# Kernel optimization log

Measured on AMD Instinct MI355X. Metric: run time of the kernel, lower is better.

## Reference

```python
import jax, jax.numpy as jnp
import numpy as np

N_WIRES = 12
N_QLAYERS = 2
DIM = 2 ** N_WIRES


def setup_inputs() -> dict:
    key = jax.random.key(0)
    k0, k1, k2, k3 = jax.random.split(key, 4)
    x = jax.random.normal(k0, (2048, 1024), dtype=jnp.float32)
    # TT cores: ranks [1,16,1], input dims [32,32], output dims [8,9]
    core0 = jax.random.normal(k1, (1, 32, 8, 16), dtype=jnp.float32) * 0.05
    core1 = jax.random.normal(k2, (16, 32, 9, 1), dtype=jnp.float32) * 0.05
    tt_bias = jnp.zeros((72,), dtype=jnp.float32)
    global_angles = jax.random.normal(k3, (N_QLAYERS, N_WIRES, 3), dtype=jnp.float32) * 0.1
    return {"x": x, "core0": core0, "core1": core1, "tt_bias": tt_bias,
            "global_angles": global_angles}


def _rot(angles):
    # angles [..., 3] -> combined U = Rz @ Ry @ Rx, shape [..., 2, 2] complex64
    half = angles * 0.5
    cx, sx = jnp.cos(half[..., 0]), jnp.sin(half[..., 0])
    cy, sy = jnp.cos(half[..., 1]), jnp.sin(half[..., 1])
    cz, sz = jnp.cos(half[..., 2]), jnp.sin(half[..., 2])
    zero = jnp.zeros_like(cx)
    cplx = jax.lax.complex
    Rx = jnp.stack([jnp.stack([cplx(cx, zero), cplx(zero, -sx)], -1),
                    jnp.stack([cplx(zero, -sx), cplx(cx, zero)], -1)], -2)
    Ry = jnp.stack([jnp.stack([cplx(cy, zero), cplx(-sy, zero)], -1),
                    jnp.stack([cplx(sy, zero), cplx(cy, zero)], -1)], -2)
    ez, ezc = cplx(cz, -sz), cplx(cz, sz)  # exp(-i z/2), exp(+i z/2)
    zc = cplx(zero, zero)
    Rz = jnp.stack([jnp.stack([ez, zc], -1), jnp.stack([zc, ezc], -1)], -2)
    return jnp.einsum('...ij,...jk,...kl->...il', Rz, Ry, Rx)


def _apply_1q(state, U, w):
    # state [bsz, 2^n]; U [bsz, 2, 2]; wire 0 = most significant qubit
    bsz = state.shape[0]
    left, right = 2 ** w, 2 ** (N_WIRES - w - 1)
    s = state.reshape(bsz, left, 2, right)
    s = jnp.einsum('bij,bljr->blir', U, s)
    return s.reshape(bsz, DIM)


def _cnot(state, c, t):
    bsz = state.shape[0]
    s = state.reshape((bsz,) + (2,) * N_WIRES)
    s0 = jax.lax.index_in_dim(s, 0, c + 1, keepdims=True)
    s1 = jax.lax.index_in_dim(s, 1, c + 1, keepdims=True)
    s1 = jnp.flip(s1, axis=t + 1)  # flip target amplitudes where control = 1
    return jnp.concatenate([s0, s1], axis=c + 1).reshape(bsz, DIM)


def reference(x, core0, core1, tt_bias, global_angles):
    bsz = x.shape[0]
    # --- TT layer: x[b,32,32] contracted with two TT cores -> [b,8,9] -> [b,72]
    x_rs = x.reshape(bsz, 32, 32)
    tt_out = jnp.einsum('bij,aipq,qjrs->bpr', x_rs, core0, core1).reshape(bsz, -1) + tt_bias
    # residual global angles
    angles = global_angles[None, :, :, :] + tt_out.reshape(bsz, N_QLAYERS, N_WIRES, 3)
    U = _rot(angles)  # [bsz, L, n, 2, 2]
    # --- tensor-product Ry encoding of x[:, :n_wires] on |0...0>
    enc = x[:, :N_WIRES] * 0.5
    amp = jnp.stack([jnp.cos(enc), jnp.sin(enc)], -1)  # [bsz, n, 2]
    state = amp[:, 0, :]
    for w in range(1, N_WIRES):
        state = (state[:, :, None] * amp[:, w, None, :]).reshape(bsz, -1)
    state = state.astype(jnp.complex64)  # [bsz, 2^n]
    # --- VQC layers: fused Rz@Ry@Rx per wire, then ring CNOT (noise_prob=0)
    for k in range(N_QLAYERS):
        for w in range(N_WIRES):
            state = _apply_1q(state, U[:, k, w], w)
        for i in range(N_WIRES - 1):
            state = _cnot(state, i, i + 1)
        state = _cnot(state, N_WIRES - 1, 0)
    # --- MeasureAll(PauliZ): <Z_w> per wire
    probs = jnp.real(state * jnp.conj(state))  # [bsz, 2^n]
    idx = jnp.arange(DIM)[:, None]
    bits = (idx >> jnp.arange(N_WIRES - 1, -1, -1)[None, :]) & 1  # [2^n, n]
    zsign = (1.0 - 2.0 * bits).astype(jnp.float32)
    return probs @ zsign  # [bsz, n_wires]
```

## Files before the change

kernel.cpp:

```cpp
#include <hip/hip_runtime.h>
#include <math.h>

#define N_WIRES 12

__host__ __device__ constexpr int parity12(int x) {
  x ^= x >> 8; x ^= x >> 4; x ^= x >> 2; x ^= x >> 1;
  return x & 1;
}

__host__ __device__ constexpr int lanemask_of(int m) {
  return (((m >> 9) & 1) << 0) | (((m >> 8) & 1) << 1) |
         (((m >> 7) & 1) << 2) | (((m >> 6) & 1) << 3) |
         (((m >> 5) & 1) << 4) | (((m >> 11) & 1) << 5);
}

typedef float2 f2;
__device__ __forceinline__ f2 mk2(float a, float b) { f2 r; r.x = a; r.y = b; return r; }
__device__ __forceinline__ f2 pkmul(f2 a, f2 b) {
  f2 d; asm("v_pk_mul_f32 %0, %1, %2" : "=v"(d) : "v"(a), "v"(b)); return d;
}
__device__ __forceinline__ f2 pkfma(f2 a, f2 b, f2 c) {
  f2 d; asm("v_pk_fma_f32 %0, %1, %2, %3" : "=v"(d) : "v"(a), "v"(b), "v"(c)); return d;
}
__device__ __forceinline__ f2 swap2(f2 v) { return mk2(v.y, v.x); }

struct cpx { float r, i; };
__device__ __forceinline__ cpx cmulc(cpx a, cpx b) {
  return {a.r * b.r - a.i * b.i, a.r * b.i + a.i * b.r};
}
__device__ __forceinline__ cpx fpick(float r0, float i0, float r1, float i1, int b) {
  cpx c; c.r = b ? r1 : r0; c.i = b ? i1 : i0; return c;
}
__device__ __forceinline__ float rl(float v, int l) {
  return __int_as_float(__builtin_amdgcn_readlane(__float_as_int(v), l));
}

template <int CTRL>
__device__ __forceinline__ float dppmov(float v) {
  return __int_as_float(
      __builtin_amdgcn_mov_dpp(__float_as_int(v), CTRL, 0xF, 0xF, true));
}

template <int LM>
__device__ __forceinline__ float lshfl(float v) {
  if constexpr (LM == 0) {
    return v;
  } else if constexpr (LM == 0x01) {
    return dppmov<0xB1>(v);
  } else if constexpr (LM == 0x02) {
    return dppmov<0x4E>(v);
  } else if constexpr (LM == 0x03) {
    return dppmov<0x1B>(v);
  } else if constexpr (LM == 0x04) {
    return dppmov<0x1B>(dppmov<0x141>(v));
  } else if constexpr (LM == 0x07) {
    return dppmov<0x141>(v);
  } else if constexpr (LM == 0x08) {
    return dppmov<0x141>(dppmov<0x140>(v));
  } else if constexpr (LM == 0x0F) {
    return dppmov<0x140>(v);
  } else if constexpr ((LM & 0x30) != 0) {
    return lshfl<LM & 0x0F>(__shfl_xor(v, LM & 0x30, 64));
  } else {
    return __shfl_xor(v, LM, 64);
  }
}
template <int LM>
__device__ __forceinline__ f2 lshfl2(f2 v) {
  return mk2(lshfl<LM>(v.x), lshfl<LM>(v.y));
}

__global__ __launch_bounds__(256) void build_w_kernel(
    const float* __restrict__ core0,
    const float* __restrict__ core1,
    float* __restrict__ Wt) {
  int idx = blockIdx.x * 256 + threadIdx.x;
  int k = idx / 72;
  int o = idx - k * 72;
  int i = k >> 5, jj = k & 31;
  int p = o / 9, r = o - p * 9;
  float acc = 0.f;
#pragma unroll
  for (int q = 0; q < 16; ++q) {
    acc += core0[(i * 8 + p) * 16 + q] * core1[(q * 32 + jj) * 9 + r];
  }
  int og = o / 9, j = o - og * 9;
  Wt[k * 96 + og * 12 + j] = acc;
}

__global__ __launch_bounds__(512, 2) void tt_gemm4(
    const float* __restrict__ x,
    const float* __restrict__ Wt,
    const float* __restrict__ bias,
    float* __restrict__ ttout) {
  __shared__ __align__(16) float ws[128 * 100];
  __shared__ __align__(16) float xs[8 * 132];
  const int t = threadIdx.x;
  const int lane = t & 63;
  const int og = t >> 6;
  const int kk = lane & 15;
  const int rq = lane >> 4;
  const int row0 = blockIdx.x * 8;

  float a0[9], a1[9];
#pragma unroll
  for (int j = 0; j < 9; ++j) { a0[j] = 0.f; a1[j] = 0.f; }

  for (int s = 0; s < 8; ++s) {
    __syncthreads();
    const float4* Wg = (const float4*)(Wt + (size_t)s * 128 * 96);
#pragma unroll
    for (int i = 0; i < 6; ++i) {
      const int idx = i * 512 + t;
      const int r = idx / 24, c = idx - r * 24;
      *(float4*)&ws[r * 100 + c * 4] = Wg[idx];
    }
    if (t < 256) {
      const int rr = t >> 5, j4 = t & 31;
      *(float4*)&xs[rr * 132 + j4 * 4] =
          *(const float4*)(x + (size_t)(row0 + rr) * 1024 + s * 128 + j4 * 4);
    }
    __syncthreads();
#pragma unroll
    for (int i = 0; i < 8; ++i) {
      const int k = kk + i * 16;
      const float4 wA = *(const float4*)&ws[k * 100 + og * 12];
      const float4 wB = *(const float4*)&ws[k * 100 + og * 12 + 4];
      const float w8 = ws[k * 100 + og * 12 + 8];
      const float x0v = xs[(rq * 2) * 132 + k];
      const float x1v = xs[(rq * 2 + 1) * 132 + k];
      a0[0] += x0v * wA.x; a0[1] += x0v * wA.y;
      a0[2] += x0v * wA.z; a0[3] += x0v * wA.w;
      a0[4] += x0v * wB.x; a0[5] += x0v * wB.y;
      a0[6] += x0v * wB.z; a0[7] += x0v * wB.w;
      a0[8] += x0v * w8;
      a1[0] += x1v * wA.x; a1[1] += x1v * wA.y;
      a1[2] += x1v * wA.z; a1[3] += x1v * wA.w;
      a1[4] += x1v * wB.x; a1[5] += x1v * wB.y;
      a1[6] += x1v * wB.z; a1[7] += x1v * wB.w;
      a1[8] += x1v * w8;
    }
  }

#pragma unroll
  for (int j = 0; j < 9; ++j) {
    a0[j] += lshfl<0x01>(a0[j]);
    a0[j] += lshfl<0x02>(a0[j]);
    a0[j] += lshfl<0x04>(a0[j]);
    a0[j] += lshfl<0x08>(a0[j]);
    a1[j] += lshfl<0x01>(a1[j]);
    a1[j] += lshfl<0x02>(a1[j]);
    a1[j] += lshfl<0x04>(a1[j]);
    a1[j] += lshfl<0x08>(a1[j]);
  }
  if (kk == 0) {
#pragma unroll
    for (int j = 0; j < 9; ++j) {
      const float bj = bias[og * 9 + j];
      ttout[(size_t)(row0 + rq * 2) * 72 + og * 9 + j] = a0[j] + bj;
      ttout[(size_t)(row0 + rq * 2 + 1) * 72 + og * 9 + j] = a1[j] + bj;
    }
  }
}

template <int MASK, int ROW>
__device__ __forceinline__ void gate9(f2 R[16], f2 I[16],
    float u00r, float u00i, float u01r, float u01i,
    f2* __restrict__ buf, int t, int lane, int wq) {
  constexpr int RM   = MASK & 0x1F;
  constexpr int LMP  = lanemask_of(MASK);
  constexpr int WB   = (MASK >> 10) & 1;
  constexpr int ROWL = lanemask_of(ROW);
  constexpr int RWB  = (ROW >> 10) & 1;
  constexpr int FLIP = parity12(ROW & 3);
  constexpr int JX = (RM == 0) ? 0 : (((RM & 1) ? (RM ^ 3) : RM) >> 1);
  constexpr bool SW = (RM & 1) != 0;

  const int tsgn = ((__popc(ROWL & lane) ^ (RWB & wq)) & 1) << 31;
  const float dEi = __int_as_float(__float_as_int(u00i) ^ tsgn);
  const float oEr = __int_as_float(__float_as_int(u01r) ^ tsgn);
  const float ndEi = -dEi, noEr = -oEr;
  const f2 A  = mk2(u00r, u00r);
  const f2 C  = mk2(u01i, u01i);
  const f2 nC = mk2(-u01i, -u01i);

  auto Dof = [&](int pe, int ph) { return mk2(pe ? ndEi : dEi, ph ? ndEi : dEi); };
  auto Oof = [&](int pe, int ph) { return mk2(pe ? noEr : oEr, ph ? noEr : oEr); };

  auto upd = [&](int j, f2 Rb, f2 Ib, f2& outR, f2& outI) {
    const int pe = parity12(ROW & (2 * j));
    const int ph = pe ^ FLIP;
    const f2 Dj = Dof(pe, ph), nDj = Dof(!pe, !ph), Oj = Oof(pe, ph);
    const f2 a = R[j], ii = I[j];
    outR = pkfma(A, a, pkfma(nDj, ii, pkfma(Oj, Rb, pkmul(nC, Ib))));
    outI = pkfma(Dj, a, pkfma(A, ii, pkfma(C, Rb, pkmul(Oj, Ib))));
  };

  if constexpr (WB) {
    static_assert(RM == 0, "wave-crossing gate must have no reg part");
    const int tp = t ^ 64 ^ LMP;
#pragma unroll
    for (int ph2 = 0; ph2 < 2; ++ph2) {
      __syncthreads();
#pragma unroll
      for (int j = 0; j < 8; ++j) {
        buf[(j * 2 + 0) * 256 + t] = R[ph2 * 8 + j];
        buf[(j * 2 + 1) * 256 + t] = I[ph2 * 8 + j];
      }
      __syncthreads();
#pragma unroll
      for (int j = 0; j < 8; ++j) {
        const f2 Rb = buf[(j * 2 + 0) * 256 + tp];
        const f2 Ib = buf[(j * 2 + 1) * 256 + tp];
        upd(ph2 * 8 + j, Rb, Ib, R[ph2 * 8 + j], I[ph2 * 8 + j]);
      }
    }
  } else if constexpr (LMP != 0 && RM == 0) {
#pragma unroll
    for (int j = 0; j < 16; ++j) {
      const f2 Rb = lshfl2<LMP>(R[j]);
      const f2 Ib = lshfl2<LMP>(I[j]);
      f2 nR, nI;
      upd(j, Rb, Ib, nR, nI);
      R[j] = nR; I[j] = nI;
    }
  } else if constexpr (LMP != 0 && RM != 0) {
#pragma unroll
    for (int j = 0; j < 16; ++j) {
      const int j2 = j ^ JX;
      if (j < j2) {
        f2 Rb1 = lshfl2<LMP>(R[j2]), Ib1 = lshfl2<LMP>(I[j2]);
        f2 Rb2 = lshfl2<LMP>(R[j]),  Ib2 = lshfl2<LMP>(I[j]);
        if constexpr (SW) {
          Rb1 = swap2(Rb1); Ib1 = swap2(Ib1);
          Rb2 = swap2(Rb2); Ib2 = swap2(Ib2);
        }
        f2 nR1, nI1, nR2, nI2;
        upd(j, Rb1, Ib1, nR1, nI1);
        upd(j2, Rb2, Ib2, nR2, nI2);
        R[j] = nR1; I[j] = nI1; R[j2] = nR2; I[j2] = nI2;
      }
    }
  } else {
#pragma unroll
    for (int j = 0; j < 16; ++j) {
      const int j2 = j ^ JX;
      if (j < j2) {
        f2 Rb1 = R[j2], Ib1 = I[j2], Rb2 = R[j], Ib2 = I[j];
        if constexpr (SW) {
          Rb1 = swap2(Rb1); Ib1 = swap2(Ib1);
          Rb2 = swap2(Rb2); Ib2 = swap2(Ib2);
        }
        f2 nR1, nI1, nR2, nI2;
        upd(j, Rb1, Ib1, nR1, nI1);
        upd(j2, Rb2, Ib2, nR2, nI2);
        R[j] = nR1; I[j] = nI1; R[j2] = nR2; I[j2] = nI2;
      }
    }
  }
}

__global__ __launch_bounds__(256, 3) void vqc_kernel10(
    const float* __restrict__ x,
    const float* __restrict__ ttout,
    const float* __restrict__ gang,
    float* __restrict__ out) {
  const int t = threadIdx.x;
  const int lane = t & 63;
  const int wq = (t >> 6) & 1;
  const int row = t >> 7;
  const int b = blockIdx.x * 2 + row;
  const float* ttb = ttout + (size_t)b * 72;

  __shared__ __align__(16) f2 buf[4096];

  float c0 = 0.f, c1 = 0.f, c2 = 0.f, c3 = 0.f;
  const bool uLane = lane < 12;
  const bool fLane = (lane >= 16) && (lane < 28);
  if (uLane || fLane) {
    const int w = uLane ? lane : lane - 16;
    const int k = uLane ? 1 : 0;
    const int gbase = (k * 12 + w) * 3;
    const int tbase = k * 36 + w * 3;
    const float a0 = gang[gbase + 0] + ttb[tbase + 0];
    const float a1 = gang[gbase + 1] + ttb[tbase + 1];
    const float a2 = gang[gbase + 2] + ttb[tbase + 2];
    const float cx = cosf(0.5f * a0), sx = sinf(0.5f * a0);
    const float cy = cosf(0.5f * a1), sy = sinf(0.5f * a1);
    const float cz = cosf(0.5f * a2), sz = sinf(0.5f * a2);
    const float m00r = cy * cx,   m00i = sy * sx;
    const float m01r = -sy * cx,  m01i = -cy * sx;
    const float m10r = sy * cx,   m10i = -cy * sx;
    const float m11r = cy * cx,   m11i = -sy * sx;
    const float U00r = cz * m00r + sz * m00i, U00i = cz * m00i - sz * m00r;
    const float U01r = cz * m01r + sz * m01i, U01i = cz * m01i - sz * m01r;
    const float U10r = cz * m10r - sz * m10i, U10i = cz * m10i + sz * m10r;
    const float U11r = cz * m11r - sz * m11i, U11i = cz * m11i + sz * m11r;
    if (uLane) {
      c0 = U00r; c1 = U00i; c2 = U01r; c3 = U01i;
    } else {
      const float e = x[(size_t)b * 1024 + w] * 0.5f;
      const float cc = cosf(e), ss = sinf(e);
      c0 = U00r * cc + U01r * ss;  c1 = U00i * cc + U01i * ss;
      c2 = U10r * cc + U11r * ss;  c3 = U10i * cc + U11i * ss;
    }
  }

  const int bw0 = (lane >> 5) & 1;
  const int bw1 = (wq ^ lane) & 1;
  const int bw2 = (lane ^ (lane >> 1)) & 1;
  const int bw3 = ((lane >> 1) ^ (lane >> 2)) & 1;
  const int bw4 = ((lane >> 2) ^ (lane >> 3)) & 1;
  const int bw5 = ((lane >> 3) ^ (lane >> 4)) & 1;
  const int l4 = (lane >> 4) & 1;

  cpx P = fpick(rl(c0, 16), rl(c1, 16), rl(c2, 16), rl(c3, 16), bw0);
  P = cmulc(P, fpick(rl(c0, 17), rl(c1, 17), rl(c2, 17), rl(c3, 17), bw1));
  P = cmulc(P, fpick(rl(c0, 18), rl(c1, 18), rl(c2, 18), rl(c3, 18), bw2));
  P = cmulc(P, fpick(rl(c0, 19), rl(c1, 19), rl(c2, 19), rl(c3, 19), bw3));
  P = cmulc(P, fpick(rl(c0, 20), rl(c1, 20), rl(c2, 20), rl(c3, 20), bw4));
  P = cmulc(P, fpick(rl(c0, 21), rl(c1, 21), rl(c2, 21), rl(c3, 21), bw5));

  cpx PT[8];
  {
    const cpx F6a = fpick(rl(c0, 22), rl(c1, 22), rl(c2, 22), rl(c3, 22), l4);
    const cpx F6b = fpick(rl(c0, 22), rl(c1, 22), rl(c2, 22), rl(c3, 22), l4 ^ 1);
    cpx F7[2], F8[2];
    F7[0] = {rl(c0, 23), rl(c1, 23)};  F7[1] = {rl(c2, 23), rl(c3, 23)};
    F8[0] = {rl(c0, 24), rl(c1, 24)};  F8[1] = {rl(c2, 24), rl(c3, 24)};
    const cpx P6a = cmulc(P, F6a), P6b = cmulc(P, F6b);
    cpx t67[4];
#pragma unroll
    for (int i = 0; i < 4; ++i) {
      const int r4 = i >> 1, r3 = i & 1;
      t67[i] = cmulc(r4 ? P6b : P6a, F7[r4 ^ r3]);
    }
#pragma unroll
    for (int i = 0; i < 8; ++i) {
      const int r3 = (i >> 1) & 1, r2 = i & 1;
      PT[i] = cmulc(t67[i >> 1], F8[r3 ^ r2]);
    }
  }

  cpx TLo[8];
  {
    cpx F9[2], F10[2], F11[2];
    F9[0]  = {rl(c0, 25), rl(c1, 25)};  F9[1]  = {rl(c2, 25), rl(c3, 25)};
    F10[0] = {rl(c0, 26), rl(c1, 26)};  F10[1] = {rl(c2, 26), rl(c3, 26)};
    F11[0] = {rl(c0, 27), rl(c1, 27)};  F11[1] = {rl(c2, 27), rl(c3, 27)};
    cpx t01[4];
#pragma unroll
    for (int i = 0; i < 4; ++i) {
      const int r1 = i >> 1, r0 = i & 1;
      t01[i] = cmulc(F10[r1 ^ r0], F11[r0]);
    }
#pragma unroll
    for (int i = 0; i < 8; ++i) {
      const int r2 = i >> 2, r1 = (i >> 1) & 1;
      TLo[i] = cmulc(F9[r2 ^ r1], t01[i & 3]);
    }
  }

  f2 R[16], I[16];
#pragma unroll
  for (int j = 0; j < 16; ++j) {
    const cpx Av = PT[j >> 1];
    const int il = (2 * j) & 7;
    const f2 Tre = mk2(TLo[il].r, TLo[il ^ 3].r);
    const f2 Tim = mk2(TLo[il].i, TLo[il ^ 3].i);
    const f2 Ar = mk2(Av.r, Av.r);
    R[j] = pkfma(mk2(-Av.i, -Av.i), Tim, pkmul(Ar, Tre));
    I[j] = pkfma(mk2(Av.i, Av.i), Tre, pkmul(Ar, Tim));
  }

#define GATE(MASK, ROW, G)                                                  \
  gate9<MASK, ROW>(R, I, rl(c0, G), rl(c1, G), rl(c2, G), rl(c3, G),        \
                   buf, t, lane, wq)

  GATE(0xC00, 0x400, 0);
  GATE(0x200, 0xE00, 1);
  GATE(0x100, 0xD00, 2);
  GATE(0x080, 0xC80, 3);
  GATE(0x040, 0xC40, 4);
  GATE(0x020, 0xC20, 5);
  GATE(0x010, 0xC10, 6);
  GATE(0x008, 0xC08, 7);
  GATE(0x004, 0xC04, 8);
  GATE(0x002, 0xC02, 9);
  GATE(0x001, 0xC01, 10);
  GATE(0xBFF, 0xC00, 11);
#undef GATE

  constexpr int MROWS[12] = {0xFFF, 0xA00, 0x700, 0xB80, 0x7C0, 0xBE0,
                             0x7F0, 0xBF8, 0x7FC, 0xBFE, 0x7FF, 0xBFF};
  const f2 Spp = mk2(1.f, 1.f),  Smm = mk2(-1.f, -1.f);
  const f2 Spm = mk2(1.f, -1.f), Smp = mk2(-1.f, 1.f);
  f2 acc2[12];
#pragma unroll
  for (int w = 0; w < 12; ++w) acc2[w] = mk2(0.f, 0.f);
#pragma unroll
  for (int j = 0; j < 16; ++j) {
    const f2 pr2 = pkfma(I[j], I[j], pkmul(R[j], R[j]));
#pragma unroll
    for (int w = 0; w < 12; ++w) {
      const int sl = parity12(MROWS[w] & (2 * j));
      const int sh = sl ^ parity12(MROWS[w] & 3);
      const f2 S = sl ? (sh ? Smm : Smp) : (sh ? Spm : Spp);
      acc2[w] = pkfma(S, pr2, acc2[w]);
    }
  }
  __syncthreads();
  float* sred = (float*)buf;
#pragma unroll
  for (int w = 0; w < 12; ++w) {
    float v = acc2[w].x + acc2[w].y;
    const int sg = (__popc(lanemask_of(MROWS[w]) & lane) ^
                    (wq & ((MROWS[w] >> 10) & 1))) & 1;
    if (sg) v = -v;
    v += lshfl<0x01>(v);
    v += lshfl<0x02>(v);
    v += lshfl<0x04>(v);
    v += lshfl<0x08>(v);
    v += __shfl_xor(v, 16, 64);
    v += __shfl_xor(v, 32, 64);
    if (lane == 0) sred[(t >> 6) * 12 + w] = v;
  }
  __syncthreads();
  if (t < 24) {
    const int rr = t / 12, w = t - rr * 12;
    out[(size_t)(blockIdx.x * 2 + rr) * 12 + w] =
        sred[(rr * 2) * 12 + w] + sred[(rr * 2 + 1) * 12 + w];
  }
}

extern "C" void kernel_launch(void* const* d_in, const int* in_sizes, int n_in,
                              void* d_out, int out_size, void* d_ws, size_t ws_size,
                              hipStream_t stream) {
  const float* x       = (const float*)d_in[0];
  const float* core0   = (const float*)d_in[1];
  const float* core1   = (const float*)d_in[2];
  const float* tt_bias = (const float*)d_in[3];
  const float* gang    = (const float*)d_in[4];
  float* out = (float*)d_out;
  float* Wt     = (float*)d_ws;
  float* ttout  = (float*)d_ws + 98304;

  const int bsz = in_sizes[0] / 1024;

  build_w_kernel<<<288, 256, 0, stream>>>(core0, core1, Wt);
  tt_gemm4<<<bsz / 8, 512, 0, stream>>>(x, Wt, tt_bias, ttout);
  vqc_kernel10<<<bsz / 2, 256, 0, stream>>>(x, ttout, gang, out);
}
```

Before: 50.78 us.

## Map one batch row per wavefront with 32 register amplitudes, dropping LDS exchanges

Each 4096-amplitude state vector now lives in one 64-lane wavefront holding 32 complex pairs per lane. Before, the state was split across two waves with 16 pairs each. This removes the shared-memory exchange and the block barriers for the wave-crossing gate and the final cross-wave reduction. Each wave writes its result directly. The cost is doubled register pressure, so launch bounds drop to 2 blocks per SIMD, which lowers occupancy and risks spills.

```diff
diff --git a/kernel.cpp b/kernel.cpp
--- a/kernel.cpp
+++ b/kernel.cpp
@@ -11,7 +11,7 @@
 __host__ __device__ constexpr int lanemask_of(int m) {
   return (((m >> 9) & 1) << 0) | (((m >> 8) & 1) << 1) |
          (((m >> 7) & 1) << 2) | (((m >> 6) & 1) << 3) |
-         (((m >> 5) & 1) << 4) | (((m >> 11) & 1) << 5);
+         (((m >> 10) & 1) << 4) | (((m >> 11) & 1) << 5);
 }
 
 typedef float2 f2;
@@ -164,19 +164,16 @@
 }
 
 template <int MASK, int ROW>
-__device__ __forceinline__ void gate9(f2 R[16], f2 I[16],
-    float u00r, float u00i, float u01r, float u01i,
-    f2* __restrict__ buf, int t, int lane, int wq) {
-  constexpr int RM   = MASK & 0x1F;
+__device__ __forceinline__ void gate11(f2 R[32], f2 I[32],
+    float u00r, float u00i, float u01r, float u01i, int lane) {
+  constexpr int RM   = MASK & 0x3F;
   constexpr int LMP  = lanemask_of(MASK);
-  constexpr int WB   = (MASK >> 10) & 1;
   constexpr int ROWL = lanemask_of(ROW);
-  constexpr int RWB  = (ROW >> 10) & 1;
   constexpr int FLIP = parity12(ROW & 3);
   constexpr int JX = (RM == 0) ? 0 : (((RM & 1) ? (RM ^ 3) : RM) >> 1);
   constexpr bool SW = (RM & 1) != 0;
 
-  const int tsgn = ((__popc(ROWL & lane) ^ (RWB & wq)) & 1) << 31;
+  const int tsgn = (__popc(ROWL & lane) & 1) << 31;
   const float dEi = __int_as_float(__float_as_int(u00i) ^ tsgn);
   const float oEr = __int_as_float(__float_as_int(u01r) ^ tsgn);
   const float ndEi = -dEi, noEr = -oEr;
@@ -196,28 +193,9 @@
     outI = pkfma(Dj, a, pkfma(A, ii, pkfma(C, Rb, pkmul(Oj, Ib))));
   };
 
-  if constexpr (WB) {
-    static_assert(RM == 0, "wave-crossing gate must have no reg part");
-    const int tp = t ^ 64 ^ LMP;
-#pragma unroll
-    for (int ph2 = 0; ph2 < 2; ++ph2) {
-      __syncthreads();
-#pragma unroll
-      for (int j = 0; j < 8; ++j) {
-        buf[(j * 2 + 0) * 256 + t] = R[ph2 * 8 + j];
-        buf[(j * 2 + 1) * 256 + t] = I[ph2 * 8 + j];
-      }
-      __syncthreads();
-#pragma unroll
-      for (int j = 0; j < 8; ++j) {
-        const f2 Rb = buf[(j * 2 + 0) * 256 + tp];
-        const f2 Ib = buf[(j * 2 + 1) * 256 + tp];
-        upd(ph2 * 8 + j, Rb, Ib, R[ph2 * 8 + j], I[ph2 * 8 + j]);
-      }
-    }
-  } else if constexpr (LMP != 0 && RM == 0) {
-#pragma unroll
-    for (int j = 0; j < 16; ++j) {
+  if constexpr (LMP != 0 && RM == 0) {
+#pragma unroll
+    for (int j = 0; j < 32; ++j) {
       const f2 Rb = lshfl2<LMP>(R[j]);
       const f2 Ib = lshfl2<LMP>(I[j]);
       f2 nR, nI;
@@ -226,7 +204,7 @@
     }
   } else if constexpr (LMP != 0 && RM != 0) {
 #pragma unroll
-    for (int j = 0; j < 16; ++j) {
+    for (int j = 0; j < 32; ++j) {
       const int j2 = j ^ JX;
       if (j < j2) {
         f2 Rb1 = lshfl2<LMP>(R[j2]), Ib1 = lshfl2<LMP>(I[j2]);
@@ -243,7 +221,7 @@
     }
   } else {
 #pragma unroll
-    for (int j = 0; j < 16; ++j) {
+    for (int j = 0; j < 32; ++j) {
       const int j2 = j ^ JX;
       if (j < j2) {
         f2 Rb1 = R[j2], Ib1 = I[j2], Rb2 = R[j], Ib2 = I[j];
@@ -260,19 +238,15 @@
   }
 }
 
-__global__ __launch_bounds__(256, 3) void vqc_kernel10(
+__global__ __launch_bounds__(256, 2) void vqc_kernel11(
     const float* __restrict__ x,
     const float* __restrict__ ttout,
     const float* __restrict__ gang,
     float* __restrict__ out) {
   const int t = threadIdx.x;
   const int lane = t & 63;
-  const int wq = (t >> 6) & 1;
-  const int row = t >> 7;
-  const int b = blockIdx.x * 2 + row;
+  const int b = blockIdx.x * 4 + (t >> 6);
   const float* ttb = ttout + (size_t)b * 72;
-
-  __shared__ __align__(16) f2 buf[4096];
 
   float c0 = 0.f, c1 = 0.f, c2 = 0.f, c3 = 0.f;
   const bool uLane = lane < 12;
@@ -307,75 +281,79 @@
   }
 
   const int bw0 = (lane >> 5) & 1;
-  const int bw1 = (wq ^ lane) & 1;
+  const int bw1 = ((lane >> 4) ^ lane) & 1;
   const int bw2 = (lane ^ (lane >> 1)) & 1;
   const int bw3 = ((lane >> 1) ^ (lane >> 2)) & 1;
   const int bw4 = ((lane >> 2) ^ (lane >> 3)) & 1;
-  const int bw5 = ((lane >> 3) ^ (lane >> 4)) & 1;
-  const int l4 = (lane >> 4) & 1;
+  const int l3v = (lane >> 3) & 1;
 
   cpx P = fpick(rl(c0, 16), rl(c1, 16), rl(c2, 16), rl(c3, 16), bw0);
   P = cmulc(P, fpick(rl(c0, 17), rl(c1, 17), rl(c2, 17), rl(c3, 17), bw1));
   P = cmulc(P, fpick(rl(c0, 18), rl(c1, 18), rl(c2, 18), rl(c3, 18), bw2));
   P = cmulc(P, fpick(rl(c0, 19), rl(c1, 19), rl(c2, 19), rl(c3, 19), bw3));
   P = cmulc(P, fpick(rl(c0, 20), rl(c1, 20), rl(c2, 20), rl(c3, 20), bw4));
-  P = cmulc(P, fpick(rl(c0, 21), rl(c1, 21), rl(c2, 21), rl(c3, 21), bw5));
 
   cpx PT[8];
   {
-    const cpx F6a = fpick(rl(c0, 22), rl(c1, 22), rl(c2, 22), rl(c3, 22), l4);
-    const cpx F6b = fpick(rl(c0, 22), rl(c1, 22), rl(c2, 22), rl(c3, 22), l4 ^ 1);
-    cpx F7[2], F8[2];
+    const cpx F5a = fpick(rl(c0, 21), rl(c1, 21), rl(c2, 21), rl(c3, 21), l3v);
+    const cpx F5b = fpick(rl(c0, 21), rl(c1, 21), rl(c2, 21), rl(c3, 21), l3v ^ 1);
+    cpx F6[2], F7[2];
+    F6[0] = {rl(c0, 22), rl(c1, 22)};  F6[1] = {rl(c2, 22), rl(c3, 22)};
     F7[0] = {rl(c0, 23), rl(c1, 23)};  F7[1] = {rl(c2, 23), rl(c3, 23)};
-    F8[0] = {rl(c0, 24), rl(c1, 24)};  F8[1] = {rl(c2, 24), rl(c3, 24)};
-    const cpx P6a = cmulc(P, F6a), P6b = cmulc(P, F6b);
-    cpx t67[4];
+    const cpx P5a = cmulc(P, F5a), P5b = cmulc(P, F5b);
+    cpx t56[4];
 #pragma unroll
     for (int i = 0; i < 4; ++i) {
-      const int r4 = i >> 1, r3 = i & 1;
-      t67[i] = cmulc(r4 ? P6b : P6a, F7[r4 ^ r3]);
+      const int r5 = i >> 1, r4 = i & 1;
+      t56[i] = cmulc(r5 ? P5b : P5a, F6[r5 ^ r4]);
     }
 #pragma unroll
     for (int i = 0; i < 8; ++i) {
-      const int r3 = (i >> 1) & 1, r2 = i & 1;
-      PT[i] = cmulc(t67[i >> 1], F8[r3 ^ r2]);
-    }
-  }
-
-  cpx TLo[8];
+      const int r4 = (i >> 1) & 1, r3 = i & 1;
+      PT[i] = cmulc(t56[i >> 1], F7[r4 ^ r3]);
+    }
+  }
+
+  cpx TL[16];
   {
-    cpx F9[2], F10[2], F11[2];
+    cpx F8[2], F9[2], F10[2], F11[2];
+    F8[0]  = {rl(c0, 24), rl(c1, 24)};  F8[1]  = {rl(c2, 24), rl(c3, 24)};
     F9[0]  = {rl(c0, 25), rl(c1, 25)};  F9[1]  = {rl(c2, 25), rl(c3, 25)};
     F10[0] = {rl(c0, 26), rl(c1, 26)};  F10[1] = {rl(c2, 26), rl(c3, 26)};
     F11[0] = {rl(c0, 27), rl(c1, 27)};  F11[1] = {rl(c2, 27), rl(c3, 27)};
-    cpx t01[4];
+    cpx t10[4];
 #pragma unroll
     for (int i = 0; i < 4; ++i) {
       const int r1 = i >> 1, r0 = i & 1;
-      t01[i] = cmulc(F10[r1 ^ r0], F11[r0]);
-    }
+      t10[i] = cmulc(F10[r1 ^ r0], F11[r0]);
+    }
+    cpx t9[8];
 #pragma unroll
     for (int i = 0; i < 8; ++i) {
       const int r2 = i >> 2, r1 = (i >> 1) & 1;
-      TLo[i] = cmulc(F9[r2 ^ r1], t01[i & 3]);
-    }
-  }
-
-  f2 R[16], I[16];
-#pragma unroll
-  for (int j = 0; j < 16; ++j) {
-    const cpx Av = PT[j >> 1];
-    const int il = (2 * j) & 7;
-    const f2 Tre = mk2(TLo[il].r, TLo[il ^ 3].r);
-    const f2 Tim = mk2(TLo[il].i, TLo[il ^ 3].i);
+      t9[i] = cmulc(F9[r2 ^ r1], t10[i & 3]);
+    }
+#pragma unroll
+    for (int i = 0; i < 16; ++i) {
+      const int r3 = i >> 3, r2 = (i >> 2) & 1;
+      TL[i] = cmulc(F8[r3 ^ r2], t9[i & 7]);
+    }
+  }
+
+  f2 R[32], I[32];
+#pragma unroll
+  for (int j = 0; j < 32; ++j) {
+    const cpx Av = PT[(j >> 2) & 7];
+    const int il = (2 * j) & 15;
+    const f2 Tre = mk2(TL[il].r, TL[il ^ 3].r);
+    const f2 Tim = mk2(TL[il].i, TL[il ^ 3].i);
     const f2 Ar = mk2(Av.r, Av.r);
     R[j] = pkfma(mk2(-Av.i, -Av.i), Tim, pkmul(Ar, Tre));
     I[j] = pkfma(mk2(Av.i, Av.i), Tre, pkmul(Ar, Tim));
   }
 
 #define GATE(MASK, ROW, G)                                                  \
-  gate9<MASK, ROW>(R, I, rl(c0, G), rl(c1, G), rl(c2, G), rl(c3, G),        \
-                   buf, t, lane, wq)
+  gate11<MASK, ROW>(R, I, rl(c0, G), rl(c1, G), rl(c2, G), rl(c3, G), lane)
 
   GATE(0xC00, 0x400, 0);
   GATE(0x200, 0xE00, 1);
@@ -399,7 +377,7 @@
 #pragma unroll
   for (int w = 0; w < 12; ++w) acc2[w] = mk2(0.f, 0.f);
 #pragma unroll
-  for (int j = 0; j < 16; ++j) {
+  for (int j = 0; j < 32; ++j) {
     const f2 pr2 = pkfma(I[j], I[j], pkmul(R[j], R[j]));
 #pragma unroll
     for (int w = 0; w < 12; ++w) {
@@ -409,27 +387,17 @@
       acc2[w] = pkfma(S, pr2, acc2[w]);
     }
   }
-  __syncthreads();
-  float* sred = (float*)buf;
 #pragma unroll
   for (int w = 0; w < 12; ++w) {
     float v = acc2[w].x + acc2[w].y;
-    const int sg = (__popc(lanemask_of(MROWS[w]) & lane) ^
-                    (wq & ((MROWS[w] >> 10) & 1))) & 1;
-    if (sg) v = -v;
+    if (__popc(lanemask_of(MROWS[w]) & lane) & 1) v = -v;
     v += lshfl<0x01>(v);
     v += lshfl<0x02>(v);
     v += lshfl<0x04>(v);
     v += lshfl<0x08>(v);
     v += __shfl_xor(v, 16, 64);
     v += __shfl_xor(v, 32, 64);
-    if (lane == 0) sred[(t >> 6) * 12 + w] = v;
-  }
-  __syncthreads();
-  if (t < 24) {
-    const int rr = t / 12, w = t - rr * 12;
-    out[(size_t)(blockIdx.x * 2 + rr) * 12 + w] =
-        sred[(rr * 2) * 12 + w] + sred[(rr * 2 + 1) * 12 + w];
+    if (lane == 0) out[(size_t)b * 12 + w] = v;
   }
 }
 
@@ -449,5 +417,5 @@
 
   build_w_kernel<<<288, 256, 0, stream>>>(core0, core1, Wt);
   tt_gemm4<<<bsz / 8, 512, 0, stream>>>(x, Wt, tt_bias, ttout);
-  vqc_kernel10<<<bsz / 2, 256, 0, stream>>>(x, ttout, gang, out);
-}
+  vqc_kernel11<<<bsz / 4, 256, 0, stream>>>(x, ttout, gang, out);
+}
```

New measurement: 50.30 us. About the same (-0.9%).
